# Performance work log

Measured on AMD Instinct MI355X. Metric: run time of the kernel, lower is better.

Reference implementation:

```python
import jax, jax.numpy as jnp
import numpy as np

N, K, BINS, DIM = 32, 16, 100, 2
LAST_TIME = 1.0
PRIOR_LAMBDA = 1.0e5
T_INIT, T_LAST = 1.0, 2.0
JITTER = 1e-5
EPS = 1e-12


def _b_kernel(t1, t2, ls, x0_c):
    """RBF kernel between train bin centers t2 (rows) and query times t1 (cols),
    with an independent x0 block prepended (block_diag). Returns (len(t2)+1, len(t1)+1)."""
    tm = t1[None, :] - t2[:, None]                      # (P, M)
    ker = jnp.exp(-0.5 * (tm / ls[0]) ** 2)
    P, M = ker.shape
    top = jnp.concatenate([x0_c ** 2, jnp.zeros((M,), ker.dtype)])[None, :]   # (1, M+1)
    bot = jnp.concatenate([jnp.zeros((P, 1), ker.dtype), ker], axis=1)        # (P, M+1)
    return jnp.concatenate([top, bot], axis=0)


def setup_inputs() -> dict:
    key = jax.random.key(0)
    ks = jax.random.split(key, 7)
    return {
        "x0": jax.random.normal(ks[0], (N, DIM), jnp.float32),
        "v": 0.1 * jax.random.normal(ks[1], (BINS, N, DIM), jnp.float32),
        "beta": jax.random.normal(ks[2], (N,), jnp.float32),
        "prior_sigma": 0.1 + 0.9 * jax.random.uniform(ks[3], (1,), jnp.float32),
        "prior_B_x0_c": 0.5 + jax.random.uniform(ks[4], (1,), jnp.float32),
        "prior_B_ls": 0.1 + 0.4 * jax.random.uniform(ks[5], (1,), jnp.float32),
        "prior_C_Q": 0.1 * jax.random.normal(ks[6], (N, K), jnp.float32),
        "sample_size": 100,
    }


def reference(x0, v, beta, prior_sigma, prior_B_x0_c, prior_B_ls, prior_C_Q, sample_size):
    bounds = jnp.linspace(0.0, LAST_TIME, BINS + 1)
    centers = 0.5 * (bounds[1:] + bounds[:-1])           # (BINS,)

    # ---- __compute_inv_train_cov (Woodbury via Kronecker factors) ----
    Bk = _b_kernel(centers, centers, prior_B_ls, prior_B_x0_c)          # (BINS+1, BINS+1)
    B_factor = jnp.linalg.cholesky(Bk + JITTER * jnp.eye(BINS + 1, dtype=Bk.dtype))
    C_factor = prior_C_Q                                                 # (N, K)
    D_factor = jnp.eye(DIM, dtype=x0.dtype)

    sigma_sq = jnp.clip(prior_sigma, 5.0 / BINS, None)[0] ** 2
    sigma_sq_inv = 1.0 / sigma_sq
    lambda_sq = PRIOR_LAMBDA ** 2
    reduced_dim = K * (BINS + 1) * DIM
    final_dim = N * (BINS + 1) * DIM

    R = jnp.eye(reduced_dim, dtype=x0.dtype) + sigma_sq_inv * jnp.kron(
        B_factor.T @ B_factor, jnp.kron(C_factor.T @ C_factor, D_factor.T @ D_factor))
    R_factor = jnp.linalg.cholesky(R)
    R_factor_inv = jnp.linalg.inv(R_factor).T
    K_factor = jnp.kron(B_factor, jnp.kron(C_factor, D_factor))          # (final_dim, reduced_dim)
    f = sigma_sq_inv * (K_factor @ R_factor_inv)
    inv_train_cov = (1.0 / lambda_sq) * (sigma_sq_inv * jnp.eye(final_dim, dtype=x0.dtype) - f @ f.T)

    # ---- get_v_pred / get_x_pred (noise term omitted for determinism) ----
    ts = jnp.linspace(T_INIT, T_LAST, sample_size)[:-1]                  # (T,)
    delta_t = ts[1] - ts[0]
    T = sample_size - 1

    B_cross = _b_kernel(ts, centers, prior_B_ls, prior_B_x0_c)[:, 1:]    # (BINS+1, T)
    CCt = C_factor @ C_factor.T                                          # (N, N)
    test_train_cov = lambda_sq * jnp.kron(B_cross, jnp.kron(CCt, D_factor @ D_factor.T))  # (final_dim, T*N*DIM)

    x0v = jnp.concatenate([x0.reshape(-1), v.reshape(-1)])               # (final_dim,)
    pred_v = ((test_train_cov.T @ inv_train_cov) @ x0v).reshape(T, N, DIM)

    bin_width = LAST_TIME / BINS
    x_last = x0 + bin_width * v.sum(axis=0)                              # (N, DIM)
    xt = x_last[None] + (ts - LAST_TIME)[:, None, None] * pred_v         # (T, N, DIM)

    # ---- intensity integral ----
    beta_mat = beta[:, None] + beta[None, :]                             # (N, N)
    sq = jnp.sum((xt[:, :, None, :] - xt[:, None, :, :]) ** 2, axis=-1)  # (T, N, N)
    dist = jnp.sqrt(jnp.maximum(sq, EPS))
    lambda_pred = jnp.sum(jnp.exp(beta_mat[None] - dist), axis=0) * delta_t
    return lambda_pred
```

## Files before the change

kernel.cpp:

```cpp
#include <hip/hip_runtime.h>
#include <math.h>

#define NBINS 100
#define NN    32
#define KD    16
#define NT    99

#define OFF_H   0
#define OFF_QT  3200
#define OFF_XL  3712

template<int CTRL>
__device__ __forceinline__ float fmov_dpp(float x) {
  return __int_as_float(
      __builtin_amdgcn_update_dpp(0, __float_as_int(x), CTRL, 0xf, 0xf, true));
}
__device__ __forceinline__ float frdlane(float x, int lane) {
  return __int_as_float(__builtin_amdgcn_readlane(__float_as_int(x), lane));
}
__device__ __forceinline__ float fshup(float x, float c0, int lane) {
  float v = fmov_dpp<0x111>(x);
  float x15 = frdlane(x, 15), x31 = frdlane(x, 31), x47 = frdlane(x, 47);
  v = (lane == 0)  ? c0  : v;
  v = (lane == 16) ? x15 : v;
  v = (lane == 32) ? x31 : v;
  v = (lane == 48) ? x47 : v;
  return v;
}
__device__ __forceinline__ float frdpos(float lo, float hi, int k) {
  return (k < 64) ? frdlane(lo, k) : frdlane(hi, k - 64);
}
__device__ __forceinline__ float frcp(float x) {
  float r = __builtin_amdgcn_rcpf(x);
  return r * (2.0f - x * r);
}

#define RD_LO(lo, hi, idx)  frdlane(lo, idx)
#define RD_MIX(lo, hi, idx) frdpos(lo, hi, ((idx) <= 99 ? (idx) : 99))

#define FWD_STEP(RD)                                                     \
  {                                                                      \
    float iuk = frcp(uk);                                                \
    Lrow[l * 101 + k] = u_lo * iuk;                                      \
    if (hiv) Lrow[ahi * 101 + k] = u_hi * iuk;                           \
    float dk = P * iuk * iuk;                                            \
    sdl = (l == k)   ? dk : sdl;                                         \
    sdh = (ahi == k) ? dk : sdh;                                         \
    float a0 = r0k * iuk, a1 = r1k * iuk;                                \
    float r0k1 = RD(r0_lo, r0_hi, k + 1);                                \
    float r1k1 = RD(r1_lo, r1_hi, k + 1);                                \
    float uk2  = RD(u_lo, u_hi, k + 2);                                  \
    float vk3  = RD(v_lo, v_hi, k + 3);                                  \
    if (l > k)   { r0_lo -= a0 * u_lo; r1_lo -= a1 * u_lo; }             \
    if (ahi > k) { r0_hi -= a0 * u_hi; r1_hi -= a1 * u_hi; }             \
    r0k = r0k1 - a0 * uk1;                                               \
    r1k = r1k1 - a1 * uk1;                                               \
    float g = vk1 * iuk;                                                 \
    float u63 = frdlane(u_lo, 63);                                       \
    float u1_lo = fshup(u_lo, 0.0f, l);                                  \
    float u1_hi = fshup(u_hi, u63, l);                                   \
    u_lo = u1_lo - g * v_lo;  u_hi = u1_hi - g * v_hi;                   \
    v_lo = v_lo - g * u1_lo;  v_hi = v_hi - g * u1_hi;                   \
    P *= (1.0f - g * g);                                                 \
    float uk_n  = uk  - g * vk1;                                         \
    float uk1_n = uk1 - g * vk2;                                         \
    float vk1_n = vk2 - g * uk1;                                         \
    float vk2_n = vk3 - g * uk2;                                         \
    uk = uk_n; uk1 = uk1_n; vk1 = vk1_n; vk2 = vk2_n;                    \
  }

__global__ __launch_bounds__(128) void k1_all(
    const float* __restrict__ x0, const float* __restrict__ v_in,
    const float* __restrict__ sigma_in, const float* __restrict__ ls_in,
    const float* __restrict__ Cq, float* __restrict__ ws)
{
  extern __shared__ float fsm[];
  float* Lrow  = fsm;
  float* vT    = Lrow + 100 * 101;
  float* QTl   = vT + 64 * 101;
  __shared__ float A[16 * 17], Vv[16 * 17];
  __shared__ float csC[16], csS[16];
  __shared__ float CqS[NN * KD];

  const int tid = threadIdx.x;
  const int l = tid & 63;
  const int wv = tid >> 6;
  const int j = blockIdx.x;
  const int r = l >> 2, c0 = l & 3;
  const float ls = ls_in[0];
  const float i2 = -0.5f / (ls * ls);
  float sig = fmaxf(sigma_in[0], 0.05f);
  const double sinvd = 1.0 / ((double)sig * (double)sig);
  const float sinvf = (float)sinvd;
  const int ahi = 64 + l;
  const bool hiv = (ahi < 100);

  float c = 0.0f;

  if (wv == 1) {
    for (int p = 0; p < NBINS; ++p) vT[l * 101 + p] = v_in[p * 64 + l];
    if (j == 0) {
      float acc = 0.f;
      for (int p = 0; p < NBINS; ++p) acc += vT[l * 101 + p];
      ws[OFF_XL + l] = x0[l] + 0.01f * acc;
    }
  } else {
    for (int e = l; e < NN * KD; e += 64) CqS[e] = Cq[e];
    #pragma unroll
    for (int k = 0; k < 4; ++k) {
      int ci = c0 + 4 * k;
      float acc = 0.f;
      for (int n = 0; n < NN; ++n)
        acc += CqS[n * 16 + r] * CqS[n * 16 + ci];
      A[r * 17 + ci] = acc;
      Vv[r * 17 + ci] = (r == ci) ? 1.0f : 0.0f;
    }

    for (int sweep = 0; sweep < 4; ++sweep)
    for (int m = 1; m <= 15; ++m) {
      const int hb = 31 - __clz(m);
      const int lowm = (1 << hb) - 1;
      if (l < 8) {
        int p = ((l & ~lowm) << 1) | (l & lowm), q = p ^ m;
        float app = A[p * 17 + p], aqq = A[q * 17 + q], apq = A[p * 17 + q];
        float cc = 1.0f, ss = 0.0f;
        if (fabsf(apq) > 1e-30f) {
          float th = (aqq - app) * 0.5f * __builtin_amdgcn_rcpf(apq);
          float t_ = __builtin_amdgcn_rcpf(fabsf(th) + sqrtf(th * th + 1.0f));
          t_ = (th >= 0.0f) ? t_ : -t_;
          cc = __builtin_amdgcn_rsqf(t_ * t_ + 1.0f);
          ss = t_ * cc;
        }
        csC[p] = cc; csS[p] = -ss;
        csC[q] = cc; csS[q] = ss;
      }
      const int rh = r ^ m;
      float ar = csC[r], br = csS[r];
      float nA[4], nV[4];
      #pragma unroll
      for (int k = 0; k < 4; ++k) {
        int ci = c0 + 4 * k, ch = ci ^ m;
        float ac = csC[ci], bc = csS[ci];
        float a_rc = A[r * 17 + ci],  a_hc = A[rh * 17 + ci];
        float a_rh = A[r * 17 + ch],  a_hh = A[rh * 17 + ch];
        float v_rc = Vv[r * 17 + ci], v_rh = Vv[r * 17 + ch];
        nA[k] = ac * (ar * a_rc + br * a_hc) + bc * (ar * a_rh + br * a_hh);
        nV[k] = ac * v_rc + bc * v_rh;
      }
      #pragma unroll
      for (int k = 0; k < 4; ++k) {
        int ci = c0 + 4 * k;
        A[r * 17 + ci] = nA[k];
        Vv[r * 17 + ci] = nV[k];
      }
    }

    float muj = A[j * 17 + j];
    if (muj < 0.f) muj = 0.f;
    c = (float)(sinvd * (double)muj);
    if (j == 0) {
      for (int e = l; e < 512; e += 64) {
        int jq = e >> 5, n = e & 31;
        float acc = 0.f;
        for (int k2 = 0; k2 < 16; ++k2)
          acc += CqS[n * 16 + k2] * Vv[k2 * 17 + jq];
        QTl[e] = acc;
        ws[OFF_QT + e] = acc;
      }
    } else if (l < 32) {
      float acc = 0.f;
      for (int k2 = 0; k2 < 16; ++k2)
        acc += CqS[l * 16 + k2] * Vv[k2 * 17 + j];
      QTl[j * 32 + l] = acc;
    }
  }

  __syncthreads();
  if (wv == 1) return;

  float s0l = 0.f, s1l = 0.f, s0h = 0.f, s1h = 0.f;
  for (int n = 0; n < NN; ++n) {
    float qv = QTl[j * 32 + n];
    s0l += qv * vT[(2 * n) * 101 + l];
    s1l += qv * vT[(2 * n + 1) * 101 + l];
    if (hiv) {
      s0h += qv * vT[(2 * n) * 101 + ahi];
      s1h += qv * vT[(2 * n + 1) * 101 + ahi];
    }
  }

  const float m0  = 1.0f + c * (1.0f + 1e-5f);
  const float im0 = frcp(m0);
  float gl = expf((0.01f * (float)l) * (0.01f * (float)l) * i2);
  float gh = expf((0.01f * (float)ahi) * (0.01f * (float)ahi) * i2);
  float u_lo = (l == 0) ? 1.0f : c * gl * im0;
  float u_hi = hiv ? c * gh * im0 : 0.0f;
  float v_lo = (l == 0) ? 0.0f : u_lo;
  float v_hi = u_hi;
  float r0_lo = s0l * im0, r1_lo = s1l * im0;
  float r0_hi = hiv ? s0h * im0 : 0.0f;
  float r1_hi = hiv ? s1h * im0 : 0.0f;
  float P = 1.0f;
  float sdl = 0.f, sdh = 0.f;

  float uk  = frdlane(u_lo, 0);
  float uk1 = frdlane(u_lo, 1);
  float vk1 = frdlane(v_lo, 1);
  float vk2 = frdlane(v_lo, 2);
  float r0k = frdlane(r0_lo, 0);
  float r1k = frdlane(r1_lo, 0);

  for (int k = 0; k < 60; ++k)  FWD_STEP(RD_LO)
  for (int k = 60; k < 99; ++k) FWD_STEP(RD_MIX)
  {
    const int k = 99;
    float iuk = frcp(uk);
    Lrow[l * 101 + k] = u_lo * iuk;
    if (hiv) Lrow[ahi * 101 + k] = u_hi * iuk;
    float dk = P * iuk * iuk;
    sdh = (ahi == k) ? dk : sdh;
  }

  float x0_lo = r0_lo * sdl, x1_lo = r1_lo * sdl;
  float x0_hi = r0_hi * sdh, x1_hi = r1_hi * sdh;

  float Ll = Lrow[99 * 101 + l];
  float Lh = hiv ? Lrow[99 * 101 + ahi] : 0.0f;
  for (int k = 99; k >= 1; --k) {
    float nLl = Lrow[(k - 1) * 101 + l];
    float nLh = hiv ? Lrow[(k - 1) * 101 + ahi] : 0.0f;
    float xk0 = frdpos(x0_lo, x0_hi, k);
    float xk1 = frdpos(x1_lo, x1_hi, k);
    if (l < k)   { x0_lo -= xk0 * Ll; x1_lo -= xk1 * Ll; }
    if (ahi < k) { x0_hi -= xk0 * Lh; x1_hi -= xk1 * Lh; }
    Ll = nLl; Lh = nLh;
  }

  ws[OFF_H + l * 32 + j * 2 + 0] = sinvf * x0_lo;
  ws[OFF_H + l * 32 + j * 2 + 1] = sinvf * x1_lo;
  if (hiv) {
    ws[OFF_H + ahi * 32 + j * 2 + 0] = sinvf * x0_hi;
    ws[OFF_H + ahi * 32 + j * 2 + 1] = sinvf * x1_hi;
  }
}

#define L_H   0
#define L_QT  3200
#define L_XL  3712
#define L_BC  3776
#define L_Z   13676
#define L_XT  16844
#define L_PS  23180
#define L_TOT 23436

__global__ __launch_bounds__(256) void k_tail(
    const float* __restrict__ ls_in, const float* __restrict__ beta,
    const float* __restrict__ ws, float* __restrict__ out)
{
  extern __shared__ float lds[];
  const int tid = threadIdx.x;
  const float ls = ls_in[0];
  const float i2 = -0.5f / (ls * ls);

  for (int e = tid; e < 3200; e += 256) lds[L_H + e] = ws[OFF_H + e];
  for (int e = tid; e < 512; e += 256)  lds[L_QT + e] = ws[OFF_QT + e];
  if (tid < 64) lds[L_XL + tid] = ws[OFF_XL + tid];
  for (int e = tid; e < NT * NBINS; e += 256) {
    int t = e / NBINS, p = e - t * NBINS;
    float tst = 1.0f + (float)t * (1.0f / 99.0f);
    float dd = tst - ((float)p + 0.5f) * 0.01f;
    lds[L_BC + e] = expf(dd * dd * i2);
  }
  __syncthreads();

  for (int dot = tid; dot < NT * 32; dot += 256) {
    int t = dot >> 5, jd = dot & 31;
    float acc = 0.f;
    for (int p = 0; p < NBINS; ++p)
      acc += lds[L_BC + t * NBINS + p] * lds[L_H + p * 32 + jd];
    lds[L_Z + dot] = acc;
  }
  __syncthreads();

  for (int e = tid; e < NT * 64; e += 256) {
    int t = e >> 6, nd = e & 63, n = nd >> 1, d = nd & 1;
    float acc = 0.f;
    for (int jq = 0; jq < 16; ++jq)
      acc += lds[L_QT + jq * 32 + n] * lds[L_Z + t * 32 + jq * 2 + d];
    float trel = (float)t * (1.0f / 99.0f);
    lds[L_XT + e] = lds[L_XL + nd] + trel * acc;
  }
  __syncthreads();

  {
    const int pl = tid & 63, tc = tid >> 6;
    const int gp = blockIdx.x * 64 + pl;
    const int i = gp >> 5, jj = gp & 31;
    const float bsum = beta[i] + beta[jj];
    const int t0 = tc * 25, t1 = (t0 + 25 < NT) ? t0 + 25 : NT;
    float acc = 0.f;
    for (int t = t0; t < t1; ++t) {
      float2 xi = *(const float2*)&lds[L_XT + t * 64 + 2 * i];
      float2 xj = *(const float2*)&lds[L_XT + t * 64 + 2 * jj];
      float dx = xi.x - xj.x, dy = xi.y - xj.y;
      float sq = fmaxf(dx * dx + dy * dy, 1e-12f);
      acc += expf(bsum - sqrtf(sq));
    }
    lds[L_PS + tc * 64 + pl] = acc;
  }
  __syncthreads();
  if (tid < 64) {
    float s = lds[L_PS + tid] + lds[L_PS + 64 + tid]
            + lds[L_PS + 128 + tid] + lds[L_PS + 192 + tid];
    out[blockIdx.x * 64 + tid] = s * (1.0f / 99.0f);
  }
}

extern "C" void kernel_launch(void* const* d_in, const int* in_sizes, int n_in,
                              void* d_out, int out_size, void* d_ws, size_t ws_size,
                              hipStream_t stream) {
  const float* x0    = (const float*)d_in[0];
  const float* v     = (const float*)d_in[1];
  const float* beta  = (const float*)d_in[2];
  const float* sigma = (const float*)d_in[3];
  const float* ls    = (const float*)d_in[5];
  const float* Cq    = (const float*)d_in[6];
  float* out = (float*)d_out;
  float* ws  = (float*)d_ws;

  const size_t smem1 = (size_t)(100 * 101 + 64 * 101 + 512) * sizeof(float);
  k1_all<<<16, 128, smem1, stream>>>(x0, v, sigma, ls, Cq, ws);
  k_tail<<<16, 256, (size_t)L_TOT * sizeof(float), stream>>>(ls, beta, ws, out);
}
```

Baseline: 98.55 us.

## Fuse solve and tail kernels with a global atomic grid barrier

Merges the two kernels into one 256-thread kernel that uses an atomic counter in the workspace as a grid-wide barrier between the per-column Cholesky solve phase and the intensity tail phase. Two extra waves compute the B_cross exponential table during the solve phase, so that work overlaps the serial solve instead of following it. This removes the second kernel launch and its gap, but adds a memset launch, a spin-wait barrier that assumes all 16 blocks are co-resident, and a larger LDS footprint per block.

New measurement: 102.8 us. +4.3%, slower.

```diff
diff --git a/kernel.cpp b/kernel.cpp
--- a/kernel.cpp
+++ b/kernel.cpp
@@ -9,6 +9,7 @@
 #define OFF_H   0
 #define OFF_QT  3200
 #define OFF_XL  3712
+#define OFF_CTR 4096
 
 template<int CTRL>
 __device__ __forceinline__ float fmov_dpp(float x) {
@@ -69,15 +70,30 @@
     uk = uk_n; uk1 = uk1_n; vk1 = vk1_n; vk2 = vk2_n;                    \
   }
 
-__global__ __launch_bounds__(128) void k1_all(
+#define P1_LROW 0
+#define P1_VT   10100
+#define P1_QT   16564
+#define P1_BC   17076
+#define L2_H    0
+#define L2_QT   3200
+#define L2_XL   3712
+#define L2_Z    3776
+#define L2_XT   6944
+#define L2_PS   13280
+#define LDS_TOT 26976
+
+__global__ __launch_bounds__(256) void k_fused(
     const float* __restrict__ x0, const float* __restrict__ v_in,
     const float* __restrict__ sigma_in, const float* __restrict__ ls_in,
-    const float* __restrict__ Cq, float* __restrict__ ws)
+    const float* __restrict__ Cq, const float* __restrict__ beta,
+    float* __restrict__ ws, float* __restrict__ out,
+    unsigned int* __restrict__ ctr)
 {
   extern __shared__ float fsm[];
-  float* Lrow  = fsm;
-  float* vT    = Lrow + 100 * 101;
-  float* QTl   = vT + 64 * 101;
+  float* Lrow = fsm + P1_LROW;
+  float* vT   = fsm + P1_VT;
+  float* QTl  = fsm + P1_QT;
+  float* Bc   = fsm + P1_BC;
   __shared__ float A[16 * 17], Vv[16 * 17];
   __shared__ float csC[16], csS[16];
   __shared__ float CqS[NN * KD];
@@ -103,6 +119,13 @@
       float acc = 0.f;
       for (int p = 0; p < NBINS; ++p) acc += vT[l * 101 + p];
       ws[OFF_XL + l] = x0[l] + 0.01f * acc;
+    }
+  } else if (wv >= 2) {
+    for (int e = tid - 128; e < NT * NBINS; e += 128) {
+      int t = e / NBINS, p = e - t * NBINS;
+      float tst = 1.0f + (float)t * (1.0f / 99.0f);
+      float dd = tst - ((float)p + 0.5f) * 0.01f;
+      Bc[e] = expf(dd * dd * i2);
     }
   } else {
     for (int e = l; e < NN * KD; e += 64) CqS[e] = Cq[e];
@@ -176,109 +199,95 @@
   }
 
   __syncthreads();
-  if (wv == 1) return;
-
-  float s0l = 0.f, s1l = 0.f, s0h = 0.f, s1h = 0.f;
-  for (int n = 0; n < NN; ++n) {
-    float qv = QTl[j * 32 + n];
-    s0l += qv * vT[(2 * n) * 101 + l];
-    s1l += qv * vT[(2 * n + 1) * 101 + l];
+
+  if (wv == 0) {
+    float s0l = 0.f, s1l = 0.f, s0h = 0.f, s1h = 0.f;
+    for (int n = 0; n < NN; ++n) {
+      float qv = QTl[j * 32 + n];
+      s0l += qv * vT[(2 * n) * 101 + l];
+      s1l += qv * vT[(2 * n + 1) * 101 + l];
+      if (hiv) {
+        s0h += qv * vT[(2 * n) * 101 + ahi];
+        s1h += qv * vT[(2 * n + 1) * 101 + ahi];
+      }
+    }
+
+    const float m0  = 1.0f + c * (1.0f + 1e-5f);
+    const float im0 = frcp(m0);
+    float gl = expf((0.01f * (float)l) * (0.01f * (float)l) * i2);
+    float gh = expf((0.01f * (float)ahi) * (0.01f * (float)ahi) * i2);
+    float u_lo = (l == 0) ? 1.0f : c * gl * im0;
+    float u_hi = hiv ? c * gh * im0 : 0.0f;
+    float v_lo = (l == 0) ? 0.0f : u_lo;
+    float v_hi = u_hi;
+    float r0_lo = s0l * im0, r1_lo = s1l * im0;
+    float r0_hi = hiv ? s0h * im0 : 0.0f;
+    float r1_hi = hiv ? s1h * im0 : 0.0f;
+    float P = 1.0f;
+    float sdl = 0.f, sdh = 0.f;
+
+    float uk  = frdlane(u_lo, 0);
+    float uk1 = frdlane(u_lo, 1);
+    float vk1 = frdlane(v_lo, 1);
+    float vk2 = frdlane(v_lo, 2);
+    float r0k = frdlane(r0_lo, 0);
+    float r1k = frdlane(r1_lo, 0);
+
+    for (int k = 0; k < 60; ++k)  FWD_STEP(RD_LO)
+    for (int k = 60; k < 99; ++k) FWD_STEP(RD_MIX)
+    {
+      const int k = 99;
+      float iuk = frcp(uk);
+      Lrow[l * 101 + k] = u_lo * iuk;
+      if (hiv) Lrow[ahi * 101 + k] = u_hi * iuk;
+      float dk = P * iuk * iuk;
+      sdh = (ahi == k) ? dk : sdh;
+    }
+
+    float x0_lo = r0_lo * sdl, x1_lo = r1_lo * sdl;
+    float x0_hi = r0_hi * sdh, x1_hi = r1_hi * sdh;
+
+    float Ll = Lrow[99 * 101 + l];
+    float Lh = hiv ? Lrow[99 * 101 + ahi] : 0.0f;
+    for (int k = 99; k >= 1; --k) {
+      float nLl = Lrow[(k - 1) * 101 + l];
+      float nLh = hiv ? Lrow[(k - 1) * 101 + ahi] : 0.0f;
+      float xk0 = frdpos(x0_lo, x0_hi, k);
+      float xk1 = frdpos(x1_lo, x1_hi, k);
+      if (l < k)   { x0_lo -= xk0 * Ll; x1_lo -= xk1 * Ll; }
+      if (ahi < k) { x0_hi -= xk0 * Lh; x1_hi -= xk1 * Lh; }
+      Ll = nLl; Lh = nLh;
+    }
+
+    ws[OFF_H + l * 32 + j * 2 + 0] = sinvf * x0_lo;
+    ws[OFF_H + l * 32 + j * 2 + 1] = sinvf * x1_lo;
     if (hiv) {
-      s0h += qv * vT[(2 * n) * 101 + ahi];
-      s1h += qv * vT[(2 * n + 1) * 101 + ahi];
-    }
-  }
-
-  const float m0  = 1.0f + c * (1.0f + 1e-5f);
-  const float im0 = frcp(m0);
-  float gl = expf((0.01f * (float)l) * (0.01f * (float)l) * i2);
-  float gh = expf((0.01f * (float)ahi) * (0.01f * (float)ahi) * i2);
-  float u_lo = (l == 0) ? 1.0f : c * gl * im0;
-  float u_hi = hiv ? c * gh * im0 : 0.0f;
-  float v_lo = (l == 0) ? 0.0f : u_lo;
-  float v_hi = u_hi;
-  float r0_lo = s0l * im0, r1_lo = s1l * im0;
-  float r0_hi = hiv ? s0h * im0 : 0.0f;
-  float r1_hi = hiv ? s1h * im0 : 0.0f;
-  float P = 1.0f;
-  float sdl = 0.f, sdh = 0.f;
-
-  float uk  = frdlane(u_lo, 0);
-  float uk1 = frdlane(u_lo, 1);
-  float vk1 = frdlane(v_lo, 1);
-  float vk2 = frdlane(v_lo, 2);
-  float r0k = frdlane(r0_lo, 0);
-  float r1k = frdlane(r1_lo, 0);
-
-  for (int k = 0; k < 60; ++k)  FWD_STEP(RD_LO)
-  for (int k = 60; k < 99; ++k) FWD_STEP(RD_MIX)
-  {
-    const int k = 99;
-    float iuk = frcp(uk);
-    Lrow[l * 101 + k] = u_lo * iuk;
-    if (hiv) Lrow[ahi * 101 + k] = u_hi * iuk;
-    float dk = P * iuk * iuk;
-    sdh = (ahi == k) ? dk : sdh;
-  }
-
-  float x0_lo = r0_lo * sdl, x1_lo = r1_lo * sdl;
-  float x0_hi = r0_hi * sdh, x1_hi = r1_hi * sdh;
-
-  float Ll = Lrow[99 * 101 + l];
-  float Lh = hiv ? Lrow[99 * 101 + ahi] : 0.0f;
-  for (int k = 99; k >= 1; --k) {
-    float nLl = Lrow[(k - 1) * 101 + l];
-    float nLh = hiv ? Lrow[(k - 1) * 101 + ahi] : 0.0f;
-    float xk0 = frdpos(x0_lo, x0_hi, k);
-    float xk1 = frdpos(x1_lo, x1_hi, k);
-    if (l < k)   { x0_lo -= xk0 * Ll; x1_lo -= xk1 * Ll; }
-    if (ahi < k) { x0_hi -= xk0 * Lh; x1_hi -= xk1 * Lh; }
-    Ll = nLl; Lh = nLh;
-  }
-
-  ws[OFF_H + l * 32 + j * 2 + 0] = sinvf * x0_lo;
-  ws[OFF_H + l * 32 + j * 2 + 1] = sinvf * x1_lo;
-  if (hiv) {
-    ws[OFF_H + ahi * 32 + j * 2 + 0] = sinvf * x0_hi;
-    ws[OFF_H + ahi * 32 + j * 2 + 1] = sinvf * x1_hi;
-  }
-}
-
-#define L_H   0
-#define L_QT  3200
-#define L_XL  3712
-#define L_BC  3776
-#define L_Z   13676
-#define L_XT  16844
-#define L_PS  23180
-#define L_TOT 23436
-
-__global__ __launch_bounds__(256) void k_tail(
-    const float* __restrict__ ls_in, const float* __restrict__ beta,
-    const float* __restrict__ ws, float* __restrict__ out)
-{
-  extern __shared__ float lds[];
-  const int tid = threadIdx.x;
-  const float ls = ls_in[0];
-  const float i2 = -0.5f / (ls * ls);
-
-  for (int e = tid; e < 3200; e += 256) lds[L_H + e] = ws[OFF_H + e];
-  for (int e = tid; e < 512; e += 256)  lds[L_QT + e] = ws[OFF_QT + e];
-  if (tid < 64) lds[L_XL + tid] = ws[OFF_XL + tid];
-  for (int e = tid; e < NT * NBINS; e += 256) {
-    int t = e / NBINS, p = e - t * NBINS;
-    float tst = 1.0f + (float)t * (1.0f / 99.0f);
-    float dd = tst - ((float)p + 0.5f) * 0.01f;
-    lds[L_BC + e] = expf(dd * dd * i2);
-  }
+      ws[OFF_H + ahi * 32 + j * 2 + 0] = sinvf * x0_hi;
+      ws[OFF_H + ahi * 32 + j * 2 + 1] = sinvf * x1_hi;
+    }
+  }
+
+  __threadfence();
+  __syncthreads();
+  if (tid == 0) {
+    __hip_atomic_fetch_add(ctr, 1u, __ATOMIC_ACQ_REL, __HIP_MEMORY_SCOPE_AGENT);
+    while (__hip_atomic_load(ctr, __ATOMIC_ACQUIRE, __HIP_MEMORY_SCOPE_AGENT)
+           < 16u) { __builtin_amdgcn_s_sleep(1); }
+  }
+  __syncthreads();
+  __threadfence();
+
+  for (int e = tid; e < 3200; e += 256) fsm[L2_H + e] = ws[OFF_H + e];
+  for (int e = tid; e < 512; e += 256)  fsm[L2_QT + e] = ws[OFF_QT + e];
+  if (tid < 64) fsm[L2_XL + tid] = ws[OFF_XL + tid];
   __syncthreads();
 
   for (int dot = tid; dot < NT * 32; dot += 256) {
     int t = dot >> 5, jd = dot & 31;
     float acc = 0.f;
     for (int p = 0; p < NBINS; ++p)
-      acc += lds[L_BC + t * NBINS + p] * lds[L_H + p * 32 + jd];
-    lds[L_Z + dot] = acc;
+      acc += Bc[t * NBINS + p] * fsm[L2_H + p * 32 + jd];
+    fsm[L2_Z + dot] = acc;
   }
   __syncthreads();
 
@@ -286,9 +295,9 @@
     int t = e >> 6, nd = e & 63, n = nd >> 1, d = nd & 1;
     float acc = 0.f;
     for (int jq = 0; jq < 16; ++jq)
-      acc += lds[L_QT + jq * 32 + n] * lds[L_Z + t * 32 + jq * 2 + d];
+      acc += fsm[L2_QT + jq * 32 + n] * fsm[L2_Z + t * 32 + jq * 2 + d];
     float trel = (float)t * (1.0f / 99.0f);
-    lds[L_XT + e] = lds[L_XL + nd] + trel * acc;
+    fsm[L2_XT + e] = fsm[L2_XL + nd] + trel * acc;
   }
   __syncthreads();
 
@@ -300,18 +309,18 @@
     const int t0 = tc * 25, t1 = (t0 + 25 < NT) ? t0 + 25 : NT;
     float acc = 0.f;
     for (int t = t0; t < t1; ++t) {
-      float2 xi = *(const float2*)&lds[L_XT + t * 64 + 2 * i];
-      float2 xj = *(const float2*)&lds[L_XT + t * 64 + 2 * jj];
+      float2 xi = *(const float2*)&fsm[L2_XT + t * 64 + 2 * i];
+      float2 xj = *(const float2*)&fsm[L2_XT + t * 64 + 2 * jj];
       float dx = xi.x - xj.x, dy = xi.y - xj.y;
       float sq = fmaxf(dx * dx + dy * dy, 1e-12f);
       acc += expf(bsum - sqrtf(sq));
     }
-    lds[L_PS + tc * 64 + pl] = acc;
+    fsm[L2_PS + tc * 64 + pl] = acc;
   }
   __syncthreads();
   if (tid < 64) {
-    float s = lds[L_PS + tid] + lds[L_PS + 64 + tid]
-            + lds[L_PS + 128 + tid] + lds[L_PS + 192 + tid];
+    float s = fsm[L2_PS + tid] + fsm[L2_PS + 64 + tid]
+            + fsm[L2_PS + 128 + tid] + fsm[L2_PS + 192 + tid];
     out[blockIdx.x * 64 + tid] = s * (1.0f / 99.0f);
   }
 }
@@ -327,8 +336,9 @@
   const float* Cq    = (const float*)d_in[6];
   float* out = (float*)d_out;
   float* ws  = (float*)d_ws;
-
-  const size_t smem1 = (size_t)(100 * 101 + 64 * 101 + 512) * sizeof(float);
-  k1_all<<<16, 128, smem1, stream>>>(x0, v, sigma, ls, Cq, ws);
-  k_tail<<<16, 256, (size_t)L_TOT * sizeof(float), stream>>>(ls, beta, ws, out);
-}
+  unsigned int* ctr = (unsigned int*)(ws + OFF_CTR);
+
+  hipMemsetAsync(ctr, 0, sizeof(unsigned int), stream);
+  const size_t smem = (size_t)LDS_TOT * sizeof(float);
+  k_fused<<<16, 256, smem, stream>>>(x0, v, sigma, ls, Cq, beta, ws, out, ctr);
+}
```
